# Performance work log

Hardware: AMD Instinct MI355X
Metric: run time of the kernel (lower is better)

Reference implementation:

```python
import jax, jax.numpy as jnp
import numpy as np

NEG_SLOPE = 0.2


def gatv2_layer(x, src, dst, Wl, Wr, att, bias, concat):
    # PyG GATv2Conv (share_weights=False): x_l = W_l x (source), x_r = W_r x (target)
    # e_ij = att . leaky_relu(x_l[j] + x_r[i]); alpha = softmax over incoming edges at i
    N = x.shape[0]
    H, C = att.shape
    xl = (x @ Wl).reshape(N, H, C)
    xr = (x @ Wr).reshape(N, H, C)
    msg = jax.nn.leaky_relu(xl[src] + xr[dst], NEG_SLOPE)          # [E, H, C]
    logits = jnp.einsum('ehc,hc->eh', msg, att)                     # [E, H]
    mx = jax.ops.segment_max(logits, dst, num_segments=N)           # [N, H]
    ex = jnp.exp(logits - mx[dst])
    denom = jax.ops.segment_sum(ex, dst, num_segments=N)            # [N, H]
    alpha = ex / denom[dst]                                         # [E, H]
    out = jax.ops.segment_sum(alpha[:, :, None] * xl[src], dst, num_segments=N)  # [N, H, C]
    out = out.reshape(N, H * C) if concat else out.mean(axis=1)
    return out + bias


def gat_forward(x, edge_index, Wl1, Wr1, att1, b1, Wl2, Wr2, att2, b2, Wl3, Wr3, att3, b3):
    N = x.shape[0]
    loop = jnp.arange(N, dtype=edge_index.dtype)
    src = jnp.concatenate([edge_index[0], loop])  # add self loops (PyG default)
    dst = jnp.concatenate([edge_index[1], loop])
    # eval mode: feature/attention dropout are identity
    h = jax.nn.elu(gatv2_layer(x, src, dst, Wl1, Wr1, att1, b1, concat=True))
    h = jax.nn.elu(gatv2_layer(h, src, dst, Wl2, Wr2, att2, b2, concat=True))
    return gatv2_layer(h, src, dst, Wl3, Wr3, att3, b3, concat=False)


def setup_inputs() -> dict:
    key = jax.random.key(0)
    ks = jax.random.split(key, 16)
    N, E = 50000, 800000
    IN, HID, H, OUT = 256, 32, 8, 64
    D1 = HID * H  # 256
    s = 0.05
    return {
        'x': jax.random.normal(ks[0], (N, IN), dtype=jnp.float32),
        'edge_index': jax.random.randint(ks[1], (2, E), 0, N, dtype=jnp.int64),
        'Wl1': jax.random.normal(ks[2], (IN, D1), dtype=jnp.float32) * s,
        'Wr1': jax.random.normal(ks[3], (IN, D1), dtype=jnp.float32) * s,
        'att1': jax.random.normal(ks[4], (H, HID), dtype=jnp.float32) * s,
        'b1': jnp.zeros((D1,), dtype=jnp.float32),
        'Wl2': jax.random.normal(ks[5], (D1, D1), dtype=jnp.float32) * s,
        'Wr2': jax.random.normal(ks[6], (D1, D1), dtype=jnp.float32) * s,
        'att2': jax.random.normal(ks[7], (H, HID), dtype=jnp.float32) * s,
        'b2': jnp.zeros((D1,), dtype=jnp.float32),
        'Wl3': jax.random.normal(ks[8], (D1, OUT), dtype=jnp.float32) * s,
        'Wr3': jax.random.normal(ks[9], (D1, OUT), dtype=jnp.float32) * s,
        'att3': jax.random.normal(ks[10], (1, OUT), dtype=jnp.float32) * s,
        'b3': jnp.zeros((OUT,), dtype=jnp.float32),
    }


def reference(x, edge_index, Wl1, Wr1, att1, b1, Wl2, Wr2, att2, b2, Wl3, Wr3, att3, b3):
    return gat_forward(x, edge_index, Wl1, Wr1, att1, b1, Wl2, Wr2, att2, b2, Wl3, Wr3, att3, b3)
```

## Files before the change

### kernel.cpp

```cpp
#include <hip/hip_runtime.h>
#include <hip/hip_fp16.h>

#define NEG_SLOPE 0.2f

typedef __attribute__((ext_vector_type(8))) _Float16 f16x8;
typedef __attribute__((ext_vector_type(2))) _Float16 f16x2;
typedef __attribute__((ext_vector_type(4))) float f32x4;

__device__ __forceinline__ void gload_lds16(const unsigned short* g, unsigned short* lds) {
    __builtin_amdgcn_global_load_lds(
        (const __attribute__((address_space(1))) void*)g,
        (__attribute__((address_space(3))) void*)lds, 16, 0, 0);
}

__device__ __forceinline__ f16x2 habs2(f16x2 v) {
    unsigned int u = __builtin_bit_cast(unsigned int, v) & 0x7FFF7FFFu;
    return __builtin_bit_cast(f16x2, u);
}


__global__ void detect_i64_kernel(const unsigned int* __restrict__ w, int E, int* __restrict__ flag) {
    __shared__ unsigned int ssum[256];
    int n = E < 4096 ? E : 4096;
    unsigned int local = 0;
    for (int k = threadIdx.x; k < n; k += 256) local |= w[2 * k + 1];
    ssum[threadIdx.x] = local;
    __syncthreads();
    for (int off = 128; off > 0; off >>= 1) {
        if (threadIdx.x < off) ssum[threadIdx.x] |= ssum[threadIdx.x + off];
        __syncthreads();
    }
    if (threadIdx.x == 0) flag[0] = (ssum[0] == 0) ? 1 : 0;
}

__global__ void count_deg_kernel(const void* __restrict__ eiv, int E,
                                 const int* __restrict__ flag, int* __restrict__ deg) {
    int e = blockIdx.x * blockDim.x + threadIdx.x;
    if (e >= E) return;
    int d;
    if (*flag) d = (int)((const long long*)eiv)[(size_t)E + e];
    else       d = ((const int*)eiv)[(size_t)E + e];
    atomicAdd(&deg[d], 1);
}

__global__ void scan_block_kernel(const int* __restrict__ deg, int* __restrict__ row_ptr,
                                  int* __restrict__ partial, int N) {
    __shared__ int sd[1024];
    int t = threadIdx.x;
    int g = blockIdx.x * 1024 + t;
    int v = (g < N) ? deg[g] : 0;
    sd[t] = v;
    __syncthreads();
    for (int off = 1; off < 1024; off <<= 1) {
        int add = (t >= off) ? sd[t - off] : 0;
        __syncthreads();
        sd[t] += add;
        __syncthreads();
    }
    if (g < N) row_ptr[g + 1] = sd[t];
    if (t == 1023) partial[blockIdx.x] = sd[1023];
    if (g == 0) row_ptr[0] = 0;
}

__global__ void scan_top_kernel(int* __restrict__ partial, int nb) {
    if (threadIdx.x == 0 && blockIdx.x == 0) {
        int run = 0;
        for (int j = 0; j < nb; ++j) { run += partial[j]; partial[j] = run; }
    }
}

__global__ void scan_addoff_kernel(int* __restrict__ row_ptr, const int* __restrict__ partial, int N) {
    int g = blockIdx.x * 256 + threadIdx.x;
    if (g >= N) return;
    int b = g >> 10;
    if (b > 0) row_ptr[g + 1] += partial[b - 1];
}

__global__ void scatter_kernel(const void* __restrict__ eiv, int E,
                               const int* __restrict__ flag,
                               const int* __restrict__ row_ptr,
                               int* __restrict__ cursor, int* __restrict__ csr) {
    int e = blockIdx.x * blockDim.x + threadIdx.x;
    if (e >= E) return;
    int s, d;
    if (*flag) {
        s = (int)((const long long*)eiv)[e];
        d = (int)((const long long*)eiv)[(size_t)E + e];
    } else {
        s = ((const int*)eiv)[e];
        d = ((const int*)eiv)[(size_t)E + e];
    }
    int pos = atomicAdd(&cursor[d], 1);
    csr[row_ptr[d] + pos] = s;
}


__global__ void to_f16_kernel(const float* __restrict__ src, int n4,
                              unsigned short* __restrict__ dst) {
    int i = blockIdx.x * blockDim.x + threadIdx.x;
    if (i >= n4) return;
    float4 v = *reinterpret_cast<const float4*>(&src[(size_t)i * 4]);
    ushort4 h;
    h.x = __half_as_ushort(__float2half(v.x));
    h.y = __half_as_ushort(__float2half(v.y));
    h.z = __half_as_ushort(__float2half(v.z));
    h.w = __half_as_ushort(__float2half(v.w));
    *reinterpret_cast<ushort4*>(&dst[(size_t)i * 4]) = h;
}

__global__ void splitT_w_kernel(const float* __restrict__ Wl, const float* __restrict__ Wr, int M,
                                unsigned short* __restrict__ WT) {
    int k = blockIdx.x;
    int m2 = blockIdx.y * 256 + threadIdx.x;
    if (m2 >= 2 * M) return;
    float v = (m2 < M) ? Wl[(size_t)k * M + m2] : Wr[(size_t)k * M + (m2 - M)];
    WT[(size_t)m2 * 256 + k] = __half_as_ushort(__float2half(v));
}


__global__ __launch_bounds__(256) void gemm_mfma_kernel(
    const unsigned short* __restrict__ A, const unsigned short* __restrict__ B,
    __half* __restrict__ xl16, float* __restrict__ xr32, int N, int M) {
    __shared__ unsigned short sA[128 * 64];
    __shared__ unsigned short sB[128 * 64];

    int t = threadIdx.x;
    int lane = t & 63;
    int w = t >> 6;
    int wr = (w >> 1) * 64;
    int wc = (w & 1) * 64;
    int row0 = blockIdx.x * 128;
    int n0 = blockIdx.y * 128;

    int l15 = lane & 15;
    int l4 = lane >> 4;

    int lr8 = lane >> 3;
    int lc8 = lane & 7;
    int ksw = (lc8 ^ lr8) * 8;

    f32x4 acc[4][4] = {};

    for (int k0 = 0; k0 < 256; k0 += 64) {
        __syncthreads();
        #pragma unroll
        for (int i = 0; i < 4; ++i) {
            int brow = i * 32 + w * 8;
            int row = brow + lr8;
            int ar = row0 + row; if (ar >= N) ar = N - 1;
            int bc = n0 + row;
            gload_lds16(&A[(size_t)ar * 256 + k0 + ksw], &sA[brow * 64]);
            gload_lds16(&B[(size_t)bc * 256 + k0 + ksw], &sB[brow * 64]);
        }
        __syncthreads();

        #pragma unroll
        for (int ksub = 0; ksub < 2; ++ksub) {
            int kb = ksub * 32 + l4 * 8;
            f16x8 b[4];
            #pragma unroll
            for (int fc = 0; fc < 4; ++fc) {
                int cc = wc + fc * 16 + l15;
                b[fc] = *reinterpret_cast<const f16x8*>(&sB[cc * 64 + (kb ^ ((cc & 7) << 3))]);
            }
            #pragma unroll
            for (int fr = 0; fr < 4; ++fr) {
                int r = wr + fr * 16 + l15;
                f16x8 a = *reinterpret_cast<const f16x8*>(&sA[r * 64 + (kb ^ ((r & 7) << 3))]);
                #pragma unroll
                for (int fc = 0; fc < 4; ++fc) {
                    acc[fr][fc] = __builtin_amdgcn_mfma_f32_16x16x32_f16(a, b[fc], acc[fr][fc], 0, 0, 0);
                }
            }
        }
    }

    #pragma unroll
    for (int fr = 0; fr < 4; ++fr) {
        #pragma unroll
        for (int j = 0; j < 4; ++j) {
            int row = row0 + wr + fr * 16 + l4 * 4 + j;
            if (row < N) {
                #pragma unroll
                for (int fc = 0; fc < 4; ++fc) {
                    int col = n0 + wc + fc * 16 + l15;
                    float v = acc[fr][fc][j];
                    if (col < M) xl16[(size_t)row * M + col] = __float2half(v);
                    else         xr32[(size_t)row * M + (col - M)] = v;
                }
            }
        }
    }
}


__global__ __launch_bounds__(256) void agg_h8_kernel(
    const __half* __restrict__ xl16, const float* __restrict__ xr32,
    const float* __restrict__ att, const float* __restrict__ bias,
    const int* __restrict__ row_ptr, const int* __restrict__ csr,
    unsigned short* __restrict__ oh, int N) {
    int wv = threadIdx.x >> 6;
    int i = blockIdx.x * 4 + wv;
    if (i >= N) return;
    int lane = threadIdx.x & 63;
    int half = lane >> 5;
    int cb = (lane & 31) * 8;

    f16x2 r2[4], a62[4], a42[4];
    float rxr[8];
    {
        float4 r0 = *reinterpret_cast<const float4*>(&xr32[(size_t)i * 256 + cb]);
        float4 r1 = *reinterpret_cast<const float4*>(&xr32[(size_t)i * 256 + cb + 4]);
        rxr[0] = r0.x; rxr[1] = r0.y; rxr[2] = r0.z; rxr[3] = r0.w;
        rxr[4] = r1.x; rxr[5] = r1.y; rxr[6] = r1.z; rxr[7] = r1.w;
        float4 w0 = *reinterpret_cast<const float4*>(&att[cb]);
        float4 w1 = *reinterpret_cast<const float4*>(&att[cb + 4]);
        float aa[8] = {w0.x, w0.y, w0.z, w0.w, w1.x, w1.y, w1.z, w1.w};
        #pragma unroll
        for (int j = 0; j < 4; ++j) {
            r2[j]  = f16x2{(_Float16)rxr[2 * j], (_Float16)rxr[2 * j + 1]};
            a62[j] = f16x2{(_Float16)(0.6f * aa[2 * j]), (_Float16)(0.6f * aa[2 * j + 1])};
            a42[j] = f16x2{(_Float16)(0.4f * aa[2 * j]), (_Float16)(0.4f * aa[2 * j + 1])};
        }
    }

    float acc[8], l, m;
    {
        uint4 sv = *reinterpret_cast<const uint4*>(&xl16[(size_t)i * 256 + cb]);
        const f16x2* u2 = reinterpret_cast<const f16x2*>(&sv);
        float p = 0.f;
        #pragma unroll
        for (int j = 0; j < 4; ++j) {
            f16x2 v2 = u2[j] + r2[j];
            p = __builtin_amdgcn_fdot2(a62[j], v2, p, false);
            p = __builtin_amdgcn_fdot2(a42[j], habs2(v2), p, false);
        }
        p += __shfl_xor(p, 1, 4);
        p += __shfl_xor(p, 2, 4);
        m = p;
        l = half ? 0.f : 1.f;
        #pragma unroll
        for (int j = 0; j < 4; ++j) {
            acc[2 * j]     = half ? 0.f : (float)u2[j][0];
            acc[2 * j + 1] = half ? 0.f : (float)u2[j][1];
        }
    }

    int start = row_ptr[i], end = row_ptr[i + 1];

    int kk0 = start + half, kk1 = start + 2 + half;
    int s0 = (kk0 < end) ? csr[kk0] : i;
    int s1 = (kk1 < end) ? csr[kk1] : i;
    uint4 ca = *reinterpret_cast<const uint4*>(&xl16[(size_t)s0 * 256 + cb]);
    uint4 cbv = *reinterpret_cast<const uint4*>(&xl16[(size_t)s1 * 256 + cb]);

    for (int k = start; k < end; k += 4) {
        int nk0 = k + 4 + half, nk1 = k + 6 + half;
        int t0 = (nk0 < end) ? csr[nk0] : i;
        int t1 = (nk1 < end) ? csr[nk1] : i;
        uint4 na = *reinterpret_cast<const uint4*>(&xl16[(size_t)t0 * 256 + cb]);
        uint4 nb = *reinterpret_cast<const uint4*>(&xl16[(size_t)t1 * 256 + cb]);

        const f16x2* ua2 = reinterpret_cast<const f16x2*>(&ca);
        const f16x2* ub2 = reinterpret_cast<const f16x2*>(&cbv);
        float p0 = 0.f, p1 = 0.f;
        #pragma unroll
        for (int j = 0; j < 4; ++j) {
            f16x2 v0 = ua2[j] + r2[j];
            p0 = __builtin_amdgcn_fdot2(a62[j], v0, p0, false);
            p0 = __builtin_amdgcn_fdot2(a42[j], habs2(v0), p0, false);
            f16x2 v1 = ub2[j] + r2[j];
            p1 = __builtin_amdgcn_fdot2(a62[j], v1, p1, false);
            p1 = __builtin_amdgcn_fdot2(a42[j], habs2(v1), p1, false);
        }
        p0 += __shfl_xor(p0, 1, 4);
        p0 += __shfl_xor(p0, 2, 4);
        p1 += __shfl_xor(p1, 1, 4);
        p1 += __shfl_xor(p1, 2, 4);
        float e0 = (k + half < end)     ? __expf(fminf(p0 - m, 60.f)) : 0.f;
        float e1 = (k + 2 + half < end) ? __expf(fminf(p1 - m, 60.f)) : 0.f;
        l += e0 + e1;
        #pragma unroll
        for (int j = 0; j < 4; ++j) {
            acc[2 * j]     = fmaf(e0, (float)ua2[j][0], fmaf(e1, (float)ub2[j][0], acc[2 * j]));
            acc[2 * j + 1] = fmaf(e0, (float)ua2[j][1], fmaf(e1, (float)ub2[j][1], acc[2 * j + 1]));
        }

        ca = na; cbv = nb;
    }

    l += __shfl_xor(l, 32, 64);
    #pragma unroll
    for (int c = 0; c < 8; ++c) acc[c] += __shfl_xor(acc[c], 32, 64);

    if (half == 0) {
        float4 bb0 = *reinterpret_cast<const float4*>(&bias[cb]);
        float4 bb1 = *reinterpret_cast<const float4*>(&bias[cb + 4]);
        float bs[8] = {bb0.x, bb0.y, bb0.z, bb0.w, bb1.x, bb1.y, bb1.z, bb1.w};
        float inv = 1.0f / l;
        unsigned int hw[4];
        #pragma unroll
        for (int c2 = 0; c2 < 4; ++c2) {
            float r0 = fmaf(acc[2 * c2], inv, bs[2 * c2]);
            float r1 = fmaf(acc[2 * c2 + 1], inv, bs[2 * c2 + 1]);
            r0 = (r0 > 0.f) ? r0 : (__expf(r0) - 1.f);
            r1 = (r1 > 0.f) ? r1 : (__expf(r1) - 1.f);
            unsigned short h0 = __half_as_ushort(__float2half(r0));
            unsigned short h1 = __half_as_ushort(__float2half(r1));
            hw[c2] = (unsigned int)h0 | ((unsigned int)h1 << 16);
        }
        *reinterpret_cast<uint4*>(&oh[(size_t)i * 256 + cb]) = make_uint4(hw[0], hw[1], hw[2], hw[3]);
    }
}


__global__ __launch_bounds__(256) void agg_h1_kernel(
    const __half* __restrict__ xl16, const float* __restrict__ xr32,
    const float* __restrict__ att, const float* __restrict__ bias,
    const int* __restrict__ row_ptr, const int* __restrict__ csr,
    float* __restrict__ out, int N) {
    int wv = threadIdx.x >> 6;
    int i = blockIdx.x * 4 + wv;
    if (i >= N) return;
    int lane = threadIdx.x & 63;
    int es = lane >> 3;
    int cb = (lane & 7) * 8;

    f16x2 r2[4], a62[4], a42[4];
    {
        float4 r0 = *reinterpret_cast<const float4*>(&xr32[(size_t)i * 64 + cb]);
        float4 r1 = *reinterpret_cast<const float4*>(&xr32[(size_t)i * 64 + cb + 4]);
        float rr[8] = {r0.x, r0.y, r0.z, r0.w, r1.x, r1.y, r1.z, r1.w};
        float4 w0 = *reinterpret_cast<const float4*>(&att[cb]);
        float4 w1 = *reinterpret_cast<const float4*>(&att[cb + 4]);
        float aa[8] = {w0.x, w0.y, w0.z, w0.w, w1.x, w1.y, w1.z, w1.w};
        #pragma unroll
        for (int j = 0; j < 4; ++j) {
            r2[j]  = f16x2{(_Float16)rr[2 * j], (_Float16)rr[2 * j + 1]};
            a62[j] = f16x2{(_Float16)(0.6f * aa[2 * j]), (_Float16)(0.6f * aa[2 * j + 1])};
            a42[j] = f16x2{(_Float16)(0.4f * aa[2 * j]), (_Float16)(0.4f * aa[2 * j + 1])};
        }
    }

    float acc[8], l, m;
    {
        uint4 sv = *reinterpret_cast<const uint4*>(&xl16[(size_t)i * 64 + cb]);
        const f16x2* u2 = reinterpret_cast<const f16x2*>(&sv);
        float p = 0.f;
        #pragma unroll
        for (int j = 0; j < 4; ++j) {
            f16x2 v2 = u2[j] + r2[j];
            p = __builtin_amdgcn_fdot2(a62[j], v2, p, false);
            p = __builtin_amdgcn_fdot2(a42[j], habs2(v2), p, false);
        }
        p += __shfl_xor(p, 1, 8);
        p += __shfl_xor(p, 2, 8);
        p += __shfl_xor(p, 4, 8);
        m = p;
        l = es ? 0.f : 1.f;
        #pragma unroll
        for (int j = 0; j < 4; ++j) {
            acc[2 * j]     = es ? 0.f : (float)u2[j][0];
            acc[2 * j + 1] = es ? 0.f : (float)u2[j][1];
        }
    }

    int start = row_ptr[i], end = row_ptr[i + 1];

    int kk = start + es;
    int s = (kk < end) ? csr[kk] : i;
    uint4 cu = *reinterpret_cast<const uint4*>(&xl16[(size_t)s * 64 + cb]);

    for (int k = start; k < end; k += 8) {
        int nk = k + 8 + es;
        int tn = (nk < end) ? csr[nk] : i;
        uint4 nu = *reinterpret_cast<const uint4*>(&xl16[(size_t)tn * 64 + cb]);

        const f16x2* u2 = reinterpret_cast<const f16x2*>(&cu);
        float p = 0.f;
        #pragma unroll
        for (int j = 0; j < 4; ++j) {
            f16x2 v2 = u2[j] + r2[j];
            p = __builtin_amdgcn_fdot2(a62[j], v2, p, false);
            p = __builtin_amdgcn_fdot2(a42[j], habs2(v2), p, false);
        }
        p += __shfl_xor(p, 1, 8);
        p += __shfl_xor(p, 2, 8);
        p += __shfl_xor(p, 4, 8);
        float e = (k + es < end) ? __expf(fminf(p - m, 60.f)) : 0.f;
        l += e;
        #pragma unroll
        for (int j = 0; j < 4; ++j) {
            acc[2 * j]     = fmaf(e, (float)u2[j][0], acc[2 * j]);
            acc[2 * j + 1] = fmaf(e, (float)u2[j][1], acc[2 * j + 1]);
        }

        cu = nu;
    }

    l += __shfl_xor(l, 8, 64);
    l += __shfl_xor(l, 16, 64);
    l += __shfl_xor(l, 32, 64);
    #pragma unroll
    for (int c = 0; c < 8; ++c) {
        acc[c] += __shfl_xor(acc[c], 8, 64);
        acc[c] += __shfl_xor(acc[c], 16, 64);
        acc[c] += __shfl_xor(acc[c], 32, 64);
    }

    if (es == 0) {
        float inv = 1.0f / l;
        float4 bb0 = *reinterpret_cast<const float4*>(&bias[cb]);
        float4 bb1 = *reinterpret_cast<const float4*>(&bias[cb + 4]);
        float4 o0, o1;
        o0.x = fmaf(acc[0], inv, bb0.x);
        o0.y = fmaf(acc[1], inv, bb0.y);
        o0.z = fmaf(acc[2], inv, bb0.z);
        o0.w = fmaf(acc[3], inv, bb0.w);
        o1.x = fmaf(acc[4], inv, bb1.x);
        o1.y = fmaf(acc[5], inv, bb1.y);
        o1.z = fmaf(acc[6], inv, bb1.z);
        o1.w = fmaf(acc[7], inv, bb1.w);
        *reinterpret_cast<float4*>(&out[(size_t)i * 64 + cb]) = o0;
        *reinterpret_cast<float4*>(&out[(size_t)i * 64 + cb + 4]) = o1;
    }
}


extern "C" void kernel_launch(void* const* d_in, const int* in_sizes, int n_in,
                              void* d_out, int out_size, void* d_ws, size_t ws_size,
                              hipStream_t stream) {
    const float* x    = (const float*)d_in[0];
    const void*  ei   = d_in[1];
    const float* Wl1  = (const float*)d_in[2];
    const float* Wr1  = (const float*)d_in[3];
    const float* att1 = (const float*)d_in[4];
    const float* b1   = (const float*)d_in[5];
    const float* Wl2  = (const float*)d_in[6];
    const float* Wr2  = (const float*)d_in[7];
    const float* att2 = (const float*)d_in[8];
    const float* b2   = (const float*)d_in[9];
    const float* Wl3  = (const float*)d_in[10];
    const float* Wr3  = (const float*)d_in[11];
    const float* att3 = (const float*)d_in[12];
    const float* b3   = (const float*)d_in[13];
    float* out = (float*)d_out;

    int N = in_sizes[0] / 256;
    int E = in_sizes[1] / 2;

    char* w = (char*)d_ws;
    unsigned short* a16  = (unsigned short*)w; w += (size_t)N * 256 * 2;
    __half* xl16 = (__half*)w;     w += (size_t)N * 256 * 2;
    float* xr32 = (float*)w;       w += (size_t)N * 256 * sizeof(float);
    unsigned short* WT = (unsigned short*)w; w += (size_t)512 * 256 * 2;
    int* row_ptr = (int*)w; w += ((size_t)N + 2) * sizeof(int);
    int* deg     = (int*)w; w += (size_t)N * sizeof(int);
    int* csr     = (int*)w; w += (size_t)E * sizeof(int);
    int* flag    = (int*)w; w += 256;
    int* partial = (int*)w; w += 256;

    detect_i64_kernel<<<1, 256, 0, stream>>>((const unsigned int*)ei, E, flag);
    hipMemsetAsync(deg, 0, (size_t)N * sizeof(int), stream);
    count_deg_kernel<<<(E + 255) / 256, 256, 0, stream>>>(ei, E, flag, deg);
    int nb = (N + 1023) / 1024;
    scan_block_kernel<<<nb, 1024, 0, stream>>>(deg, row_ptr, partial, N);
    scan_top_kernel<<<1, 64, 0, stream>>>(partial, nb);
    scan_addoff_kernel<<<(N + 255) / 256, 256, 0, stream>>>(row_ptr, partial, N);
    hipMemsetAsync(deg, 0, (size_t)N * sizeof(int), stream);
    scatter_kernel<<<(E + 255) / 256, 256, 0, stream>>>(ei, E, flag, row_ptr, deg, csr);

    int gemm_gx = (N + 127) / 128;
    int agg_g = (N + 3) / 4;

    to_f16_kernel<<<((N * 256 / 4) + 255) / 256, 256, 0, stream>>>(x, N * 256 / 4, a16);
    splitT_w_kernel<<<dim3(256, 2), 256, 0, stream>>>(Wl1, Wr1, 256, WT);
    gemm_mfma_kernel<<<dim3(gemm_gx, 4), 256, 0, stream>>>(a16, WT, xl16, xr32, N, 256);
    agg_h8_kernel<<<agg_g, 256, 0, stream>>>(xl16, xr32, att1, b1, row_ptr, csr, a16, N);

    splitT_w_kernel<<<dim3(256, 2), 256, 0, stream>>>(Wl2, Wr2, 256, WT);
    gemm_mfma_kernel<<<dim3(gemm_gx, 4), 256, 0, stream>>>(a16, WT, xl16, xr32, N, 256);
    agg_h8_kernel<<<agg_g, 256, 0, stream>>>(xl16, xr32, att2, b2, row_ptr, csr, a16, N);

    splitT_w_kernel<<<dim3(256, 1), 256, 0, stream>>>(Wl3, Wr3, 64, WT);
    gemm_mfma_kernel<<<dim3(gemm_gx, 1), 256, 0, stream>>>(a16, WT, xl16, xr32, N, 64);
    agg_h1_kernel<<<agg_g, 256, 0, stream>>>(xl16, xr32, att3, b3, row_ptr, csr, out, N);
}
```

Measured before the change: 381.9 us.

## Store GEMM outputs as one interleaved fp16 buffer for xl and xr

The GEMM now writes both the source projection and the target projection as fp16 into a single row-interleaved buffer of width 2M, replacing the separate fp16 xl and fp32 xr arrays. The aggregation kernels read the xr half directly as fp16 with a stride of 2M. This halves xr write and read traffic and drops the per-element branch in the GEMM epilogue. The cost is a doubled row stride for the gathered xl rows, which spreads neighbour gathers over more memory, and xr is now rounded to fp16 in the GEMM, whereas before it was stored in fp32 and converted inside the aggregation kernel.

```diff
diff --git a/kernel.cpp b/kernel.cpp
--- a/kernel.cpp
+++ b/kernel.cpp
@@ -120,7 +120,7 @@
 
 __global__ __launch_bounds__(256) void gemm_mfma_kernel(
     const unsigned short* __restrict__ A, const unsigned short* __restrict__ B,
-    __half* __restrict__ xl16, float* __restrict__ xr32, int N, int M) {
+    __half* __restrict__ C16, int N, int M) {
     __shared__ unsigned short sA[128 * 64];
     __shared__ unsigned short sB[128 * 64];
 
@@ -131,6 +131,7 @@
     int wc = (w & 1) * 64;
     int row0 = blockIdx.x * 128;
     int n0 = blockIdx.y * 128;
+    int ldc = 2 * M;
 
     int l15 = lane & 15;
     int l4 = lane >> 4;
@@ -184,9 +185,7 @@
                 #pragma unroll
                 for (int fc = 0; fc < 4; ++fc) {
                     int col = n0 + wc + fc * 16 + l15;
-                    float v = acc[fr][fc][j];
-                    if (col < M) xl16[(size_t)row * M + col] = __float2half(v);
-                    else         xr32[(size_t)row * M + (col - M)] = v;
+                    C16[(size_t)row * ldc + col] = __float2half(acc[fr][fc][j]);
                 }
             }
         }
@@ -195,7 +194,7 @@
 
 
 __global__ __launch_bounds__(256) void agg_h8_kernel(
-    const __half* __restrict__ xl16, const float* __restrict__ xr32,
+    const __half* __restrict__ C16,
     const float* __restrict__ att, const float* __restrict__ bias,
     const int* __restrict__ row_ptr, const int* __restrict__ csr,
     unsigned short* __restrict__ oh, int N) {
@@ -207,18 +206,15 @@
     int cb = (lane & 31) * 8;
 
     f16x2 r2[4], a62[4], a42[4];
-    float rxr[8];
     {
-        float4 r0 = *reinterpret_cast<const float4*>(&xr32[(size_t)i * 256 + cb]);
-        float4 r1 = *reinterpret_cast<const float4*>(&xr32[(size_t)i * 256 + cb + 4]);
-        rxr[0] = r0.x; rxr[1] = r0.y; rxr[2] = r0.z; rxr[3] = r0.w;
-        rxr[4] = r1.x; rxr[5] = r1.y; rxr[6] = r1.z; rxr[7] = r1.w;
+        uint4 rv = *reinterpret_cast<const uint4*>(&C16[(size_t)i * 512 + 256 + cb]);
+        const f16x2* rp = reinterpret_cast<const f16x2*>(&rv);
         float4 w0 = *reinterpret_cast<const float4*>(&att[cb]);
         float4 w1 = *reinterpret_cast<const float4*>(&att[cb + 4]);
         float aa[8] = {w0.x, w0.y, w0.z, w0.w, w1.x, w1.y, w1.z, w1.w};
         #pragma unroll
         for (int j = 0; j < 4; ++j) {
-            r2[j]  = f16x2{(_Float16)rxr[2 * j], (_Float16)rxr[2 * j + 1]};
+            r2[j]  = rp[j];
             a62[j] = f16x2{(_Float16)(0.6f * aa[2 * j]), (_Float16)(0.6f * aa[2 * j + 1])};
             a42[j] = f16x2{(_Float16)(0.4f * aa[2 * j]), (_Float16)(0.4f * aa[2 * j + 1])};
         }
@@ -226,7 +222,7 @@
 
     float acc[8], l, m;
     {
-        uint4 sv = *reinterpret_cast<const uint4*>(&xl16[(size_t)i * 256 + cb]);
+        uint4 sv = *reinterpret_cast<const uint4*>(&C16[(size_t)i * 512 + cb]);
         const f16x2* u2 = reinterpret_cast<const f16x2*>(&sv);
         float p = 0.f;
         #pragma unroll
@@ -251,15 +247,15 @@
     int kk0 = start + half, kk1 = start + 2 + half;
     int s0 = (kk0 < end) ? csr[kk0] : i;
     int s1 = (kk1 < end) ? csr[kk1] : i;
-    uint4 ca = *reinterpret_cast<const uint4*>(&xl16[(size_t)s0 * 256 + cb]);
-    uint4 cbv = *reinterpret_cast<const uint4*>(&xl16[(size_t)s1 * 256 + cb]);
+    uint4 ca = *reinterpret_cast<const uint4*>(&C16[(size_t)s0 * 512 + cb]);
+    uint4 cbv = *reinterpret_cast<const uint4*>(&C16[(size_t)s1 * 512 + cb]);
 
     for (int k = start; k < end; k += 4) {
         int nk0 = k + 4 + half, nk1 = k + 6 + half;
         int t0 = (nk0 < end) ? csr[nk0] : i;
         int t1 = (nk1 < end) ? csr[nk1] : i;
-        uint4 na = *reinterpret_cast<const uint4*>(&xl16[(size_t)t0 * 256 + cb]);
-        uint4 nb = *reinterpret_cast<const uint4*>(&xl16[(size_t)t1 * 256 + cb]);
+        uint4 na = *reinterpret_cast<const uint4*>(&C16[(size_t)t0 * 512 + cb]);
+        uint4 nb = *reinterpret_cast<const uint4*>(&C16[(size_t)t1 * 512 + cb]);
 
         const f16x2* ua2 = reinterpret_cast<const f16x2*>(&ca);
         const f16x2* ub2 = reinterpret_cast<const f16x2*>(&cbv);
@@ -315,7 +311,7 @@
 
 
 __global__ __launch_bounds__(256) void agg_h1_kernel(
-    const __half* __restrict__ xl16, const float* __restrict__ xr32,
+    const __half* __restrict__ C16,
     const float* __restrict__ att, const float* __restrict__ bias,
     const int* __restrict__ row_ptr, const int* __restrict__ csr,
     float* __restrict__ out, int N) {
@@ -328,15 +324,14 @@
 
     f16x2 r2[4], a62[4], a42[4];
     {
-        float4 r0 = *reinterpret_cast<const float4*>(&xr32[(size_t)i * 64 + cb]);
-        float4 r1 = *reinterpret_cast<const float4*>(&xr32[(size_t)i * 64 + cb + 4]);
-        float rr[8] = {r0.x, r0.y, r0.z, r0.w, r1.x, r1.y, r1.z, r1.w};
+        uint4 rv = *reinterpret_cast<const uint4*>(&C16[(size_t)i * 128 + 64 + cb]);
+        const f16x2* rp = reinterpret_cast<const f16x2*>(&rv);
         float4 w0 = *reinterpret_cast<const float4*>(&att[cb]);
         float4 w1 = *reinterpret_cast<const float4*>(&att[cb + 4]);
         float aa[8] = {w0.x, w0.y, w0.z, w0.w, w1.x, w1.y, w1.z, w1.w};
         #pragma unroll
         for (int j = 0; j < 4; ++j) {
-            r2[j]  = f16x2{(_Float16)rr[2 * j], (_Float16)rr[2 * j + 1]};
+            r2[j]  = rp[j];
             a62[j] = f16x2{(_Float16)(0.6f * aa[2 * j]), (_Float16)(0.6f * aa[2 * j + 1])};
             a42[j] = f16x2{(_Float16)(0.4f * aa[2 * j]), (_Float16)(0.4f * aa[2 * j + 1])};
         }
@@ -344,7 +339,7 @@
 
     float acc[8], l, m;
     {
-        uint4 sv = *reinterpret_cast<const uint4*>(&xl16[(size_t)i * 64 + cb]);
+        uint4 sv = *reinterpret_cast<const uint4*>(&C16[(size_t)i * 128 + cb]);
         const f16x2* u2 = reinterpret_cast<const f16x2*>(&sv);
         float p = 0.f;
         #pragma unroll
@@ -369,12 +364,12 @@
 
     int kk = start + es;
     int s = (kk < end) ? csr[kk] : i;
-    uint4 cu = *reinterpret_cast<const uint4*>(&xl16[(size_t)s * 64 + cb]);
+    uint4 cu = *reinterpret_cast<const uint4*>(&C16[(size_t)s * 128 + cb]);
 
     for (int k = start; k < end; k += 8) {
         int nk = k + 8 + es;
         int tn = (nk < end) ? csr[nk] : i;
-        uint4 nu = *reinterpret_cast<const uint4*>(&xl16[(size_t)tn * 64 + cb]);
+        uint4 nu = *reinterpret_cast<const uint4*>(&C16[(size_t)tn * 128 + cb]);
 
         const f16x2* u2 = reinterpret_cast<const f16x2*>(&cu);
         float p = 0.f;
@@ -451,8 +446,7 @@
 
     char* w = (char*)d_ws;
     unsigned short* a16  = (unsigned short*)w; w += (size_t)N * 256 * 2;
-    __half* xl16 = (__half*)w;     w += (size_t)N * 256 * 2;
-    float* xr32 = (float*)w;       w += (size_t)N * 256 * sizeof(float);
+    __half* C16 = (__half*)w;      w += (size_t)N * 512 * 2;
     unsigned short* WT = (unsigned short*)w; w += (size_t)512 * 256 * 2;
     int* row_ptr = (int*)w; w += ((size_t)N + 2) * sizeof(int);
     int* deg     = (int*)w; w += (size_t)N * sizeof(int);
@@ -475,14 +469,14 @@
 
     to_f16_kernel<<<((N * 256 / 4) + 255) / 256, 256, 0, stream>>>(x, N * 256 / 4, a16);
     splitT_w_kernel<<<dim3(256, 2), 256, 0, stream>>>(Wl1, Wr1, 256, WT);
-    gemm_mfma_kernel<<<dim3(gemm_gx, 4), 256, 0, stream>>>(a16, WT, xl16, xr32, N, 256);
-    agg_h8_kernel<<<agg_g, 256, 0, stream>>>(xl16, xr32, att1, b1, row_ptr, csr, a16, N);
+    gemm_mfma_kernel<<<dim3(gemm_gx, 4), 256, 0, stream>>>(a16, WT, C16, N, 256);
+    agg_h8_kernel<<<agg_g, 256, 0, stream>>>(C16, att1, b1, row_ptr, csr, a16, N);
 
     splitT_w_kernel<<<dim3(256, 2), 256, 0, stream>>>(Wl2, Wr2, 256, WT);
-    gemm_mfma_kernel<<<dim3(gemm_gx, 4), 256, 0, stream>>>(a16, WT, xl16, xr32, N, 256);
-    agg_h8_kernel<<<agg_g, 256, 0, stream>>>(xl16, xr32, att2, b2, row_ptr, csr, a16, N);
+    gemm_mfma_kernel<<<dim3(gemm_gx, 4), 256, 0, stream>>>(a16, WT, C16, N, 256);
+    agg_h8_kernel<<<agg_g, 256, 0, stream>>>(C16, att2, b2, row_ptr, csr, a16, N);
 
     splitT_w_kernel<<<dim3(256, 1), 256, 0, stream>>>(Wl3, Wr3, 64, WT);
-    gemm_mfma_kernel<<<dim3(gemm_gx, 1), 256, 0, stream>>>(a16, WT, xl16, xr32, N, 64);
-    agg_h1_kernel<<<agg_g, 256, 0, stream>>>(xl16, xr32, att3, b3, row_ptr, csr, out, N);
-}
+    gemm_mfma_kernel<<<dim3(gemm_gx, 1), 256, 0, stream>>>(a16, WT, C16, N, 64);
+    agg_h1_kernel<<<agg_g, 256, 0, stream>>>(C16, att3, b3, row_ptr, csr, out, N);
+}
```

After: 362.0 us. -5.2%, faster.
